# Kernel optimization log

Measured on AMD Instinct MI355X. Metric: run time of the kernel, lower is better.

## Reference

```python
import jax, jax.numpy as jnp
import numpy as np

B, IN, H = 4096, 1024, 2048


def setup_inputs() -> dict:
    key = jax.random.key(0)
    ks = jax.random.split(key, 7)
    return {
        "x": jax.random.normal(ks[0], (B, IN), jnp.float32),
        "h": jax.random.normal(ks[1], (B, H), jnp.float32),
        "c": jax.random.normal(ks[2], (B, H), jnp.float32),
        "w_ih": jax.random.normal(ks[3], (4 * H, IN), jnp.float32) * 0.02,
        "w_hh": jax.random.normal(ks[4], (4 * H, H), jnp.float32) * 0.02,
        "b_ih": jax.random.normal(ks[5], (4 * H,), jnp.float32) * 0.02,
        "b_hh": jax.random.normal(ks[6], (4 * H,), jnp.float32) * 0.02,
    }


def reference(x, h, c, w_ih, w_hh, b_ih, b_hh):
    act = jnp.sin  # custom gate activation (Sine_activation repo)
    # Combined GEMMs: same math as the 8 separate F.linear calls.
    # gates: [B, 4H], chunk order along dim 0 of weights: f, i, ic, o
    gates = (x @ w_ih.T + b_ih) + (h @ w_hh.T + b_hh)
    f_in, i_in, ic_in, o_in = jnp.split(gates, 4, axis=-1)
    ft = jax.nn.sigmoid(f_in)
    it = jax.nn.sigmoid(i_in)
    i_cands = act(ic_in)
    ct = c * ft + i_cands * it
    ot = jax.nn.sigmoid(o_in)
    ht = ot * act(ct)
    return (ht, ct)
```

## Files before the change

kernel.cpp:

```cpp
#include <hip/hip_runtime.h>

typedef __attribute__((ext_vector_type(8))) short short8;
typedef __attribute__((ext_vector_type(4))) float f32x4;

#define BDIM 4096
#define INDIM 1024
#define HDIM 2048
#define KDIM 3072
#define NDIM 8192
#define OUT_HALF 8388608
#define NKT 96
#define ACHUNKS 1572864

__device__ __forceinline__ unsigned short f2bf(float f) {
  unsigned u = __float_as_uint(f);
  u += 0x7FFFu + ((u >> 16) & 1u);
  return (unsigned short)(u >> 16);
}

__device__ __forceinline__ float sigmoidf_(float x) {
  return 1.0f / (1.0f + __expf(-x));
}

__global__ __launch_bounds__(256) void pack_all(
    const float* __restrict__ x, const float* __restrict__ hh,
    const float* __restrict__ w_ih, const float* __restrict__ w_hh,
    const float* __restrict__ b_ih, const float* __restrict__ b_hh,
    unsigned short* __restrict__ A, unsigned short* __restrict__ W,
    float* __restrict__ bias) {
  int idx = blockIdx.x * 256 + threadIdx.x;
  if (idx < ACHUNKS) {
    int m = idx / 384;
    int k0 = (idx - m * 384) * 8;
    const float* src = (k0 < INDIM) ? (x + (size_t)m * INDIM + k0)
                                    : (hh + (size_t)m * HDIM + (k0 - INDIM));
    float4 lo = ((const float4*)src)[0];
    float4 hi = ((const float4*)src)[1];
    union { unsigned short us[8]; uint4 v; } o;
    o.us[0] = f2bf(lo.x); o.us[1] = f2bf(lo.y); o.us[2] = f2bf(lo.z); o.us[3] = f2bf(lo.w);
    o.us[4] = f2bf(hi.x); o.us[5] = f2bf(hi.y); o.us[6] = f2bf(hi.z); o.us[7] = f2bf(hi.w);
    *(uint4*)(A + (size_t)m * KDIM + k0) = o.v;
  } else {
    idx -= ACHUNKS;
    int np = idx / 384;
    int rem = idx - np * 384;
    int k0 = rem * 8;
    int j = np >> 2;
    int g = np & 3;
    int n = g * HDIM + j;
    const float* src = (k0 < INDIM) ? (w_ih + (size_t)n * INDIM + k0)
                                    : (w_hh + (size_t)n * HDIM + (k0 - INDIM));
    float4 lo = ((const float4*)src)[0];
    float4 hi = ((const float4*)src)[1];
    union { unsigned short us[8]; uint4 v; } o;
    o.us[0] = f2bf(lo.x); o.us[1] = f2bf(lo.y); o.us[2] = f2bf(lo.z); o.us[3] = f2bf(lo.w);
    o.us[4] = f2bf(hi.x); o.us[5] = f2bf(hi.y); o.us[6] = f2bf(hi.z); o.us[7] = f2bf(hi.w);
    *(uint4*)(W + (size_t)np * KDIM + k0) = o.v;
    if (rem == 0) bias[np] = b_ih[n] + b_hh[n];
  }
}

__device__ __forceinline__ void gload_lds16(const void* g, void* l) {
  __builtin_amdgcn_global_load_lds(
      (const __attribute__((address_space(1))) void*)g,
      (__attribute__((address_space(3))) void*)l, 16, 0, 0);
}

#define SB0 __builtin_amdgcn_sched_barrier(0)

__global__ __launch_bounds__(512, 2) void lstm_gemm(
    const unsigned short* __restrict__ A,
    const unsigned short* __restrict__ W,
    const float* __restrict__ bias,
    const float* __restrict__ c,
    float* __restrict__ out) {
  extern __shared__ char smem[];

  const int tid = threadIdx.x;
  const int lane = tid & 63;
  const int wid = tid >> 6;

  const int bid = blockIdx.x;
  const int local = bid >> 3;
  const int tm = (bid & 7) * 2 + (local & 1);
  const int tn = local >> 1;

  int rowA0, clA0, rowA1, clA1;
  {
    int P0 = wid * 1024 + lane * 16;
    int P1 = 8192 + wid * 1024 + lane * 16;
    int r2, cp, cg;
    r2 = P0 >> 7; cp = (P0 >> 4) & 7; cg = cp ^ (r2 & 7);
    rowA0 = r2 * 2 + (cg >> 2); clA0 = cg & 3;
    r2 = P1 >> 7; cp = (P1 >> 4) & 7; cg = cp ^ (r2 & 7);
    rowA1 = r2 * 2 + (cg >> 2); clA1 = cg & 3;
  }
  const unsigned short* gA0 = A + (size_t)(tm * 256 + rowA0) * KDIM + clA0 * 8;
  const unsigned short* gA1 = A + (size_t)(tm * 256 + rowA1) * KDIM + clA1 * 8;
  const unsigned short* gB0 = W + (size_t)(tn * 256 + rowA0) * KDIM + clA0 * 8;
  const unsigned short* gB1 = W + (size_t)(tn * 256 + rowA1) * KDIM + clA1 * 8;
  const int ldA0 = wid * 1024;
  const int ldA1 = 8192 + wid * 1024;
  const int ldB0 = 16384 + wid * 1024;
  const int ldB1 = 24576 + wid * 1024;

  const int fr = lane & 15;
  const int fq = lane >> 4;
  const int wr = wid >> 2;
  const int wc = wid & 3;
  const int frh = fr >> 1;
  const int clA = (((fr & 1) << 2) | fq) ^ frh;
  const int aconst = wr * 8192 + frh * 128 + clA * 16;
  const int bconst = 16384 + wc * 4096 + frh * 128 + clA * 16;

  f32x4 acc[8][4] = {};
  short8 af[4], ag[4], bfA[4], bfB[4];

#pragma unroll
  for (int tt = 0; tt < 3; ++tt) {
    char* lb = smem + tt * 32768;
    gload_lds16(gA0, lb + ldA0);
    gload_lds16(gA1, lb + ldA1);
    gload_lds16(gB0, lb + ldB0);
    gload_lds16(gB1, lb + ldB1);
    gA0 += 32; gA1 += 32; gB0 += 32; gB1 += 32;
  }
  asm volatile("s_waitcnt vmcnt(8)" ::: "memory");
  __builtin_amdgcn_s_barrier(); SB0;
#pragma unroll
  for (int mi = 0; mi < 4; ++mi)
    af[mi] = *(const short8*)(smem + aconst + mi * 1024);
#pragma unroll
  for (int ni = 0; ni < 4; ++ni)
    bfA[ni] = *(const short8*)(smem + bconst + ni * 1024);

#define TILE_BODY(T, VMSTR, STAGE_, PREF_, BFC, BFN)                         \
  do {                                                                       \
    const char* rb = smem + ((T) & 3) * 32768;                               \
    const char* rbn = smem + (((T) + 1) & 3) * 32768;                        \
    char* lb = smem + (((T) + 3) & 3) * 32768;                               \
    if (STAGE_) {                                                            \
      gload_lds16(gA0, lb + ldA0);                                           \
      gload_lds16(gA1, lb + ldA1);                                           \
    }                                                                        \
    _Pragma("unroll")                                                        \
    for (int mi = 0; mi < 4; ++mi)                                           \
      ag[mi] = *(const short8*)(rb + aconst + (mi + 4) * 1024);              \
    SB0;                                                                     \
    __builtin_amdgcn_s_setprio(1);                                           \
    _Pragma("unroll")                                                        \
    for (int mi = 0; mi < 4; ++mi)                                           \
      _Pragma("unroll")                                                      \
      for (int ni = 0; ni < 4; ++ni)                                         \
        acc[mi][ni] = __builtin_amdgcn_mfma_f32_16x16x32_bf16(               \
            af[mi], BFC[ni], acc[mi][ni], 0, 0, 0);                          \
    __builtin_amdgcn_s_setprio(0);                                           \
    if (STAGE_) {                                                            \
      gload_lds16(gB0, lb + ldB0);                                           \
      gload_lds16(gB1, lb + ldB1);                                           \
      gA0 += 32; gA1 += 32; gB0 += 32; gB1 += 32;                            \
    }                                                                        \
    asm volatile("s_waitcnt vmcnt(" VMSTR ") lgkmcnt(0)" ::: "memory");      \
    SB0;                                                                     \
    __builtin_amdgcn_s_barrier(); SB0;                                       \
    if (PREF_) {                                                             \
      _Pragma("unroll")                                                      \
      for (int mi = 0; mi < 4; ++mi)                                         \
        af[mi] = *(const short8*)(rbn + aconst + mi * 1024);                 \
      _Pragma("unroll")                                                      \
      for (int ni = 0; ni < 4; ++ni)                                         \
        BFN[ni] = *(const short8*)(rbn + bconst + ni * 1024);                \
    }                                                                        \
    SB0;                                                                     \
    __builtin_amdgcn_s_setprio(1);                                           \
    _Pragma("unroll")                                                        \
    for (int mi = 0; mi < 4; ++mi)                                           \
      _Pragma("unroll")                                                      \
      for (int ni = 0; ni < 4; ++ni)                                         \
        acc[mi + 4][ni] = __builtin_amdgcn_mfma_f32_16x16x32_bf16(           \
            ag[mi], BFC[ni], acc[mi + 4][ni], 0, 0, 0);                      \
    __builtin_amdgcn_s_setprio(0);                                           \
  } while (0)

  for (int t = 0; t < 92; t += 2) {
    TILE_BODY(t,     "8", true, true, bfA, bfB);
    TILE_BODY(t + 1, "8", true, true, bfB, bfA);
  }
  TILE_BODY(92, "8", true,  true,  bfA, bfB);
  TILE_BODY(93, "4", false, true,  bfB, bfA);
  TILE_BODY(94, "0", false, true,  bfA, bfB);
  TILE_BODY(95, "0", false, false, bfB, bfA);
#undef TILE_BODY

  const int jw = fr;
  const int jg = tn * 64 + wc * 16 + jw;
  const f32x4 bi = *(const f32x4*)(bias + tn * 256 + wc * 64 + jw * 4);
  float* ep = (float*)smem + wid * 1152;

#pragma unroll
  for (int mi = 0; mi < 8; ++mi) {
#pragma unroll
    for (int ni = 0; ni < 4; ++ni)
#pragma unroll
      for (int r = 0; r < 4; ++r)
        ep[(fq * 4 + r) * 68 + ni * 16 + fr] = acc[mi][ni][r];
    asm volatile("s_waitcnt lgkmcnt(0)" ::: "memory");
#pragma unroll
    for (int t4 = 0; t4 < 4; ++t4) {
      const int row = fq + t4 * 4;
      f32x4 g4 = *(const f32x4*)(ep + row * 68 + jw * 4);
      const float f_in = g4[0] + bi[0];
      const float i_in = g4[1] + bi[1];
      const float ic_in = g4[2] + bi[2];
      const float o_in = g4[3] + bi[3];
      const float ft = sigmoidf_(f_in);
      const float it = sigmoidf_(i_in);
      const float ics = __sinf(ic_in);
      const int mg = tm * 256 + wr * 128 + mi * 16 + row;
      const float cv = c[(size_t)mg * HDIM + jg];
      const float ct = cv * ft + ics * it;
      const float ot = sigmoidf_(o_in);
      const float ht = ot * __sinf(ct);
      out[(size_t)mg * HDIM + jg] = ht;
      out[OUT_HALF + (size_t)mg * HDIM + jg] = ct;
    }
    asm volatile("s_waitcnt lgkmcnt(0)" ::: "memory");
  }
}

extern "C" void kernel_launch(void* const* d_in, const int* in_sizes, int n_in,
                              void* d_out, int out_size, void* d_ws, size_t ws_size,
                              hipStream_t stream) {
  const float* x    = (const float*)d_in[0];
  const float* h    = (const float*)d_in[1];
  const float* c    = (const float*)d_in[2];
  const float* w_ih = (const float*)d_in[3];
  const float* w_hh = (const float*)d_in[4];
  const float* b_ih = (const float*)d_in[5];
  const float* b_hh = (const float*)d_in[6];
  float* out = (float*)d_out;

  char* ws = (char*)d_ws;
  unsigned short* Abf = (unsigned short*)ws;
  unsigned short* Wbf = (unsigned short*)(ws + 25165824);
  float* bias = (float*)(ws + 25165824 + 50331648);

  hipFuncSetAttribute((const void*)lstm_gemm,
                      hipFuncAttributeMaxDynamicSharedMemorySize, 131072);

  pack_all<<<18432, 256, 0, stream>>>(x, h, w_ih, w_hh, b_ih, b_hh, Abf, Wbf, bias);
  lstm_gemm<<<512, 512, 131072, stream>>>(Abf, Wbf, bias, c, out);
}
```

Measured before the change: 223.0 us.

## Load B fragments directly from global into registers, halve LDS ring

Weight (B) tiles are no longer staged through LDS. Each wave now loads its B MFMA fragments straight from global memory into registers, two tiles ahead. Only A goes through the 4-stage LDS ring, so shared memory drops from 128KB to 64KB. This removes LDS write/read traffic and bank pressure for B, but each wave in a column group now fetches its own B fragments with narrower, uncoalesced 16-byte row accesses and no reuse across the waves sharing those columns, and register pressure rises.

Result: slower. 318.9 us (+43.0%).

```diff
diff --git a/kernel.cpp b/kernel.cpp
--- a/kernel.cpp
+++ b/kernel.cpp
@@ -85,24 +85,16 @@
   const int tm = (bid & 7) * 2 + (local & 1);
   const int tn = local >> 1;
 
-  int rowA0, clA0, rowA1, clA1;
-  {
-    int P0 = wid * 1024 + lane * 16;
-    int P1 = 8192 + wid * 1024 + lane * 16;
-    int r2, cp, cg;
-    r2 = P0 >> 7; cp = (P0 >> 4) & 7; cg = cp ^ (r2 & 7);
-    rowA0 = r2 * 2 + (cg >> 2); clA0 = cg & 3;
-    r2 = P1 >> 7; cp = (P1 >> 4) & 7; cg = cp ^ (r2 & 7);
-    rowA1 = r2 * 2 + (cg >> 2); clA1 = cg & 3;
-  }
-  const unsigned short* gA0 = A + (size_t)(tm * 256 + rowA0) * KDIM + clA0 * 8;
-  const unsigned short* gA1 = A + (size_t)(tm * 256 + rowA1) * KDIM + clA1 * 8;
-  const unsigned short* gB0 = W + (size_t)(tn * 256 + rowA0) * KDIM + clA0 * 8;
-  const unsigned short* gB1 = W + (size_t)(tn * 256 + rowA1) * KDIM + clA1 * 8;
-  const int ldA0 = wid * 1024;
-  const int ldA1 = 8192 + wid * 1024;
-  const int ldB0 = 16384 + wid * 1024;
-  const int ldB1 = 24576 + wid * 1024;
+  const int r2s = tid >> 3;
+  const int cgs = (tid & 7) ^ (r2s & 7);
+  const int srowA = r2s * 2 + (cgs >> 2);
+  const unsigned short* gA = A + (size_t)(tm * 256 + srowA) * KDIM + (cgs & 3) * 8;
+  const int r2s1 = (8192 + tid * 16) >> 7;
+  const int cgs1 = (tid & 7) ^ (r2s1 & 7);
+  const int srowA1 = r2s1 * 2 + (cgs1 >> 2);
+  const unsigned short* gA1 = A + (size_t)(tm * 256 + srowA1) * KDIM + (cgs1 & 3) * 8;
+  const int ldA0 = tid * 16;
+  const int ldA1 = 8192 + tid * 16;
 
   const int fr = lane & 15;
   const int fq = lane >> 4;
@@ -111,37 +103,39 @@
   const int frh = fr >> 1;
   const int clA = (((fr & 1) << 2) | fq) ^ frh;
   const int aconst = wr * 8192 + frh * 128 + clA * 16;
-  const int bconst = 16384 + wc * 4096 + frh * 128 + clA * 16;
+
+  const unsigned short* gBf0 = W + (size_t)(tn * 256 + wc * 64 +  0 + fr) * KDIM + fq * 8;
+  const unsigned short* gBf1 = W + (size_t)(tn * 256 + wc * 64 + 16 + fr) * KDIM + fq * 8;
+  const unsigned short* gBf2 = W + (size_t)(tn * 256 + wc * 64 + 32 + fr) * KDIM + fq * 8;
+  const unsigned short* gBf3 = W + (size_t)(tn * 256 + wc * 64 + 48 + fr) * KDIM + fq * 8;
 
   f32x4 acc[8][4] = {};
   short8 af[4], ag[4], bfA[4], bfB[4];
 
 #pragma unroll
   for (int tt = 0; tt < 3; ++tt) {
-    char* lb = smem + tt * 32768;
-    gload_lds16(gA0, lb + ldA0);
-    gload_lds16(gA1, lb + ldA1);
-    gload_lds16(gB0, lb + ldB0);
-    gload_lds16(gB1, lb + ldB1);
-    gA0 += 32; gA1 += 32; gB0 += 32; gB1 += 32;
-  }
+    char* lb = smem + tt * 16384;
+    gload_lds16(gA + (size_t)tt * 32, lb + ldA0);
+    gload_lds16(gA1 + (size_t)tt * 32, lb + ldA1);
+  }
+  bfA[0] = *(const short8*)gBf0; bfA[1] = *(const short8*)gBf1;
+  bfA[2] = *(const short8*)gBf2; bfA[3] = *(const short8*)gBf3;
+  bfB[0] = *(const short8*)(gBf0 + 32); bfB[1] = *(const short8*)(gBf1 + 32);
+  bfB[2] = *(const short8*)(gBf2 + 32); bfB[3] = *(const short8*)(gBf3 + 32);
   asm volatile("s_waitcnt vmcnt(8)" ::: "memory");
   __builtin_amdgcn_s_barrier(); SB0;
 #pragma unroll
   for (int mi = 0; mi < 4; ++mi)
     af[mi] = *(const short8*)(smem + aconst + mi * 1024);
-#pragma unroll
-  for (int ni = 0; ni < 4; ++ni)
-    bfA[ni] = *(const short8*)(smem + bconst + ni * 1024);
-
-#define TILE_BODY(T, VMSTR, STAGE_, PREF_, BFC, BFN)                         \
+
+#define TILE_BODY(T, VMSTR, STAGE_, PREFA_, PREFB_, BFC, BFN)                \
   do {                                                                       \
-    const char* rb = smem + ((T) & 3) * 32768;                               \
-    const char* rbn = smem + (((T) + 1) & 3) * 32768;                        \
-    char* lb = smem + (((T) + 3) & 3) * 32768;                               \
+    const char* rb = smem + ((T) & 3) * 16384;                               \
+    const char* rbn = smem + (((T) + 1) & 3) * 16384;                        \
+    char* lb = smem + (((T) + 3) & 3) * 16384;                               \
     if (STAGE_) {                                                            \
-      gload_lds16(gA0, lb + ldA0);                                           \
-      gload_lds16(gA1, lb + ldA1);                                           \
+      gload_lds16(gA + (size_t)((T) + 3) * 32, lb + ldA0);                   \
+      gload_lds16(gA1 + (size_t)((T) + 3) * 32, lb + ldA1);                  \
     }                                                                        \
     _Pragma("unroll")                                                        \
     for (int mi = 0; mi < 4; ++mi)                                           \
@@ -155,21 +149,14 @@
         acc[mi][ni] = __builtin_amdgcn_mfma_f32_16x16x32_bf16(               \
             af[mi], BFC[ni], acc[mi][ni], 0, 0, 0);                          \
     __builtin_amdgcn_s_setprio(0);                                           \
-    if (STAGE_) {                                                            \
-      gload_lds16(gB0, lb + ldB0);                                           \
-      gload_lds16(gB1, lb + ldB1);                                           \
-      gA0 += 32; gA1 += 32; gB0 += 32; gB1 += 32;                            \
-    }                                                                        \
-    asm volatile("s_waitcnt vmcnt(" VMSTR ") lgkmcnt(0)" ::: "memory");      \
-    SB0;                                                                     \
+    SB0;                                                                     \
+    asm volatile("s_waitcnt vmcnt(" VMSTR ")" ::: "memory");                 \
+    asm volatile("s_waitcnt lgkmcnt(0)" ::: "memory");                       \
     __builtin_amdgcn_s_barrier(); SB0;                                       \
-    if (PREF_) {                                                             \
+    if (PREFA_) {                                                            \
       _Pragma("unroll")                                                      \
       for (int mi = 0; mi < 4; ++mi)                                         \
         af[mi] = *(const short8*)(rbn + aconst + mi * 1024);                 \
-      _Pragma("unroll")                                                      \
-      for (int ni = 0; ni < 4; ++ni)                                         \
-        BFN[ni] = *(const short8*)(rbn + bconst + ni * 1024);                \
     }                                                                        \
     SB0;                                                                     \
     __builtin_amdgcn_s_setprio(1);                                           \
@@ -180,16 +167,24 @@
         acc[mi + 4][ni] = __builtin_amdgcn_mfma_f32_16x16x32_bf16(           \
             ag[mi], BFC[ni], acc[mi + 4][ni], 0, 0, 0);                      \
     __builtin_amdgcn_s_setprio(0);                                           \
+    SB0;                                                                     \
+    if (PREFB_) {                                                            \
+      BFC[0] = *(const short8*)(gBf0 + (size_t)((T) + 2) * 32);              \
+      BFC[1] = *(const short8*)(gBf1 + (size_t)((T) + 2) * 32);              \
+      BFC[2] = *(const short8*)(gBf2 + (size_t)((T) + 2) * 32);              \
+      BFC[3] = *(const short8*)(gBf3 + (size_t)((T) + 2) * 32);              \
+    }                                                                        \
+    SB0;                                                                     \
   } while (0)
 
   for (int t = 0; t < 92; t += 2) {
-    TILE_BODY(t,     "8", true, true, bfA, bfB);
-    TILE_BODY(t + 1, "8", true, true, bfB, bfA);
-  }
-  TILE_BODY(92, "8", true,  true,  bfA, bfB);
-  TILE_BODY(93, "4", false, true,  bfB, bfA);
-  TILE_BODY(94, "0", false, true,  bfA, bfB);
-  TILE_BODY(95, "0", false, false, bfB, bfA);
+    TILE_BODY(t,     "6", true, true, true, bfA, bfB);
+    TILE_BODY(t + 1, "6", true, true, true, bfB, bfA);
+  }
+  TILE_BODY(92, "6", true,  true,  true,  bfA, bfB);
+  TILE_BODY(93, "0", false, true,  true,  bfB, bfA);
+  TILE_BODY(94, "0", false, true,  false, bfA, bfB);
+  TILE_BODY(95, "0", false, false, false, bfB, bfA);
 #undef TILE_BODY
 
   const int jw = fr;
@@ -246,8 +241,8 @@
   float* bias = (float*)(ws + 25165824 + 50331648);
 
   hipFuncSetAttribute((const void*)lstm_gemm,
-                      hipFuncAttributeMaxDynamicSharedMemorySize, 131072);
+                      hipFuncAttributeMaxDynamicSharedMemorySize, 65536);
 
   pack_all<<<18432, 256, 0, stream>>>(x, h, w_ih, w_hh, b_ih, b_hh, Abf, Wbf, bias);
-  lstm_gemm<<<512, 512, 131072, stream>>>(Abf, Wbf, bias, c, out);
-}
+  lstm_gemm<<<512, 512, 65536, stream>>>(Abf, Wbf, bias, c, out);
+}
```

## Pre-swizzle weights into MFMA fragment layout and load B directly to registers

Applied to the files above, without the earlier changes.

The pack kernel now writes the bf16 weight matrix in a per-tile, per-lane fragment order, so the GEMM kernel loads B operands straight from global memory into registers, two tiles ahead, instead of staging them through LDS. LDS use per block is halved (only A is staged), which cuts LDS traffic and shared memory footprint. The trade-off is that B fragments now arrive with global-load latency, covered only by register double buffering. Wait counts and the pack launch grid change to match.

Measured after the change: 242.0 us. +8.5%, slower.

```diff
diff --git a/kernel.cpp b/kernel.cpp
--- a/kernel.cpp
+++ b/kernel.cpp
@@ -11,6 +11,7 @@
 #define OUT_HALF 8388608
 #define NKT 96
 #define ACHUNKS 1572864
+#define WTHREADS 786432
 
 __device__ __forceinline__ unsigned short f2bf(float f) {
   unsigned u = __float_as_uint(f);
@@ -41,22 +42,32 @@
     o.us[4] = f2bf(hi.x); o.us[5] = f2bf(hi.y); o.us[6] = f2bf(hi.z); o.us[7] = f2bf(hi.w);
     *(uint4*)(A + (size_t)m * KDIM + k0) = o.v;
   } else {
-    idx -= ACHUNKS;
-    int np = idx / 384;
-    int rem = idx - np * 384;
-    int k0 = rem * 8;
+    int widx = idx - ACHUNKS;
+    if (widx >= WTHREADS) return;
+    int tn = widx / 24576;
+    int rr = widx - tn * 24576;
+    int T = rr >> 8;
+    int q = rr & 255;
+    int np = tn * 256 + q;
     int j = np >> 2;
     int g = np & 3;
     int n = g * HDIM + j;
+    int k0 = T * 32;
     const float* src = (k0 < INDIM) ? (w_ih + (size_t)n * INDIM + k0)
                                     : (w_hh + (size_t)n * HDIM + (k0 - INDIM));
-    float4 lo = ((const float4*)src)[0];
-    float4 hi = ((const float4*)src)[1];
-    union { unsigned short us[8]; uint4 v; } o;
-    o.us[0] = f2bf(lo.x); o.us[1] = f2bf(lo.y); o.us[2] = f2bf(lo.z); o.us[3] = f2bf(lo.w);
-    o.us[4] = f2bf(hi.x); o.us[5] = f2bf(hi.y); o.us[6] = f2bf(hi.z); o.us[7] = f2bf(hi.w);
-    *(uint4*)(W + (size_t)np * KDIM + k0) = o.v;
-    if (rem == 0) bias[np] = b_ih[n] + b_hh[n];
+    size_t cbase = ((size_t)(tn * 96 + T) << 10) + (size_t)(q >> 4) * 64 * 4 ;
+    int wc = q >> 6, ni = (q >> 4) & 3, fr = q & 15;
+    size_t chunk0 = ((size_t)(tn * 96 + T) << 10) + wc * 256 + ni * 64 + fr;
+#pragma unroll
+    for (int fq = 0; fq < 4; ++fq) {
+      float4 lo = ((const float4*)(src + fq * 8))[0];
+      float4 hi = ((const float4*)(src + fq * 8))[1];
+      union { unsigned short us[8]; uint4 v; } o;
+      o.us[0] = f2bf(lo.x); o.us[1] = f2bf(lo.y); o.us[2] = f2bf(lo.z); o.us[3] = f2bf(lo.w);
+      o.us[4] = f2bf(hi.x); o.us[5] = f2bf(hi.y); o.us[6] = f2bf(hi.z); o.us[7] = f2bf(hi.w);
+      *(uint4*)(W + ((chunk0 + fq * 16) << 3)) = o.v;
+    }
+    if (T == 0) bias[np] = b_ih[n] + b_hh[n];
   }
 }
 
@@ -97,12 +108,8 @@
   }
   const unsigned short* gA0 = A + (size_t)(tm * 256 + rowA0) * KDIM + clA0 * 8;
   const unsigned short* gA1 = A + (size_t)(tm * 256 + rowA1) * KDIM + clA1 * 8;
-  const unsigned short* gB0 = W + (size_t)(tn * 256 + rowA0) * KDIM + clA0 * 8;
-  const unsigned short* gB1 = W + (size_t)(tn * 256 + rowA1) * KDIM + clA1 * 8;
   const int ldA0 = wid * 1024;
   const int ldA1 = 8192 + wid * 1024;
-  const int ldB0 = 16384 + wid * 1024;
-  const int ldB1 = 24576 + wid * 1024;
 
   const int fr = lane & 15;
   const int fq = lane >> 4;
@@ -111,37 +118,41 @@
   const int frh = fr >> 1;
   const int clA = (((fr & 1) << 2) | fq) ^ frh;
   const int aconst = wr * 8192 + frh * 128 + clA * 16;
-  const int bconst = 16384 + wc * 4096 + frh * 128 + clA * 16;
+
+  const char* gBlane = (const char*)W +
+      (((size_t)(tn * 96) << 10) + (size_t)wc * 256 + lane) * 16;
 
   f32x4 acc[8][4] = {};
   short8 af[4], ag[4], bfA[4], bfB[4];
 
 #pragma unroll
   for (int tt = 0; tt < 3; ++tt) {
-    char* lb = smem + tt * 32768;
+    char* lb = smem + tt * 16384;
     gload_lds16(gA0, lb + ldA0);
     gload_lds16(gA1, lb + ldA1);
-    gload_lds16(gB0, lb + ldB0);
-    gload_lds16(gB1, lb + ldB1);
-    gA0 += 32; gA1 += 32; gB0 += 32; gB1 += 32;
-  }
-  asm volatile("s_waitcnt vmcnt(8)" ::: "memory");
+    gA0 += 32; gA1 += 32;
+  }
+#pragma unroll
+  for (int ni = 0; ni < 4; ++ni)
+    bfA[ni] = *(const short8*)(gBlane + ni * 1024);
+#pragma unroll
+  for (int ni = 0; ni < 4; ++ni)
+    bfB[ni] = *(const short8*)(gBlane + 16384 + ni * 1024);
+  asm volatile("s_waitcnt vmcnt(12)" ::: "memory");
   __builtin_amdgcn_s_barrier(); SB0;
 #pragma unroll
   for (int mi = 0; mi < 4; ++mi)
     af[mi] = *(const short8*)(smem + aconst + mi * 1024);
-#pragma unroll
-  for (int ni = 0; ni < 4; ++ni)
-    bfA[ni] = *(const short8*)(smem + bconst + ni * 1024);
-
-#define TILE_BODY(T, VMSTR, STAGE_, PREF_, BFC, BFN)                         \
+
+#define TILE_BODY(T, STAGE_, PREFA_, LOADB_, BFC)                            \
   do {                                                                       \
-    const char* rb = smem + ((T) & 3) * 32768;                               \
-    const char* rbn = smem + (((T) + 1) & 3) * 32768;                        \
-    char* lb = smem + (((T) + 3) & 3) * 32768;                               \
+    const char* rb = smem + ((T) & 3) * 16384;                               \
+    const char* rbn = smem + (((T) + 1) & 3) * 16384;                        \
+    char* lb = smem + (((T) + 3) & 3) * 16384;                               \
     if (STAGE_) {                                                            \
       gload_lds16(gA0, lb + ldA0);                                           \
       gload_lds16(gA1, lb + ldA1);                                           \
+      gA0 += 32; gA1 += 32;                                                  \
     }                                                                        \
     _Pragma("unroll")                                                        \
     for (int mi = 0; mi < 4; ++mi)                                           \
@@ -155,21 +166,13 @@
         acc[mi][ni] = __builtin_amdgcn_mfma_f32_16x16x32_bf16(               \
             af[mi], BFC[ni], acc[mi][ni], 0, 0, 0);                          \
     __builtin_amdgcn_s_setprio(0);                                           \
-    if (STAGE_) {                                                            \
-      gload_lds16(gB0, lb + ldB0);                                           \
-      gload_lds16(gB1, lb + ldB1);                                           \
-      gA0 += 32; gA1 += 32; gB0 += 32; gB1 += 32;                            \
-    }                                                                        \
-    asm volatile("s_waitcnt vmcnt(" VMSTR ") lgkmcnt(0)" ::: "memory");      \
-    SB0;                                                                     \
+    asm volatile("s_waitcnt vmcnt(8)" ::: "memory");                         \
+    asm volatile("s_waitcnt lgkmcnt(0)" ::: "memory");                       \
     __builtin_amdgcn_s_barrier(); SB0;                                       \
-    if (PREF_) {                                                             \
+    if (PREFA_) {                                                            \
       _Pragma("unroll")                                                      \
       for (int mi = 0; mi < 4; ++mi)                                         \
         af[mi] = *(const short8*)(rbn + aconst + mi * 1024);                 \
-      _Pragma("unroll")                                                      \
-      for (int ni = 0; ni < 4; ++ni)                                         \
-        BFN[ni] = *(const short8*)(rbn + bconst + ni * 1024);                \
     }                                                                        \
     SB0;                                                                     \
     __builtin_amdgcn_s_setprio(1);                                           \
@@ -180,16 +183,23 @@
         acc[mi + 4][ni] = __builtin_amdgcn_mfma_f32_16x16x32_bf16(           \
             ag[mi], BFC[ni], acc[mi + 4][ni], 0, 0, 0);                      \
     __builtin_amdgcn_s_setprio(0);                                           \
+    if (LOADB_) {                                                            \
+      _Pragma("unroll")                                                      \
+      for (int ni = 0; ni < 4; ++ni)                                         \
+        BFC[ni] = *(const short8*)(gBlane + (size_t)((T) + 2) * 16384 +      \
+                                   ni * 1024);                               \
+    }                                                                        \
+    SB0;                                                                     \
   } while (0)
 
   for (int t = 0; t < 92; t += 2) {
-    TILE_BODY(t,     "8", true, true, bfA, bfB);
-    TILE_BODY(t + 1, "8", true, true, bfB, bfA);
-  }
-  TILE_BODY(92, "8", true,  true,  bfA, bfB);
-  TILE_BODY(93, "4", false, true,  bfB, bfA);
-  TILE_BODY(94, "0", false, true,  bfA, bfB);
-  TILE_BODY(95, "0", false, false, bfB, bfA);
+    TILE_BODY(t,     true, true, true, bfA);
+    TILE_BODY(t + 1, true, true, true, bfB);
+  }
+  TILE_BODY(92, true,  true,  true,  bfA);
+  TILE_BODY(93, false, true,  true,  bfB);
+  TILE_BODY(94, false, true,  false, bfA);
+  TILE_BODY(95, false, false, false, bfB);
 #undef TILE_BODY
 
   const int jw = fr;
@@ -246,8 +256,8 @@
   float* bias = (float*)(ws + 25165824 + 50331648);
 
   hipFuncSetAttribute((const void*)lstm_gemm,
-                      hipFuncAttributeMaxDynamicSharedMemorySize, 131072);
-
-  pack_all<<<18432, 256, 0, stream>>>(x, h, w_ih, w_hh, b_ih, b_hh, Abf, Wbf, bias);
-  lstm_gemm<<<512, 512, 131072, stream>>>(Abf, Wbf, bias, c, out);
-}
+                      hipFuncAttributeMaxDynamicSharedMemorySize, 65536);
+
+  pack_all<<<9216, 256, 0, stream>>>(x, h, w_ih, w_hh, b_ih, b_hh, Abf, Wbf, bias);
+  lstm_gemm<<<512, 512, 65536, stream>>>(Abf, Wbf, bias, c, out);
+}
```
